# Optimization experiments

Hardware: AMD Instinct MI355X
Metric: run time of the kernel (lower is better)

The kernel has to match this reference:

```python
import jax, jax.numpy as jnp
import numpy as np

TOP_K = 2  # MoEBlock default


def setup_inputs() -> dict:
    key = jax.random.key(0)
    ks = jax.random.split(key, 7)
    B_, S, D, F, E, R = 2, 2048, 1024, 4096, 4, 4
    x  = jax.random.normal(ks[0], (B_, S, D), dtype=jnp.float32)
    Wg = jax.random.normal(ks[1], (E, D), dtype=jnp.float32) * (1.0 / np.sqrt(D))
    bg = jnp.zeros((E,), dtype=jnp.float32)
    Wi = jax.random.normal(ks[2], (F, D), dtype=jnp.float32) * (1.0 / np.sqrt(D))
    Wo = jax.random.normal(ks[3], (D, F), dtype=jnp.float32) * (1.0 / np.sqrt(F))
    A  = jax.random.normal(ks[4], (E, R, D), dtype=jnp.float32) * (1.0 / np.sqrt(D))
    Bm = jax.random.normal(ks[5], (E, F, R), dtype=jnp.float32) * 0.01
    return {"x": x, "Wg": Wg, "bg": bg, "Wi": Wi, "Wo": Wo, "A": A, "B": Bm}


def reference(x, Wg, bg, Wi, Wo, A, B):
    E = Wg.shape[0]
    # ---- Router: softmax gate + top-k ----
    logits = jnp.einsum('bsd,ed->bse', x, Wg) + bg          # [B,S,E]
    scores = jax.nn.softmax(logits, axis=-1)
    topv, topi = jax.lax.top_k(scores, TOP_K)               # [B,S,K]
    # per-token combine weight for each expert (sum of matching top-k probs)
    w = jnp.sum(jax.nn.one_hot(topi, E, dtype=x.dtype) * topv[..., None], axis=-2)  # [B,S,E]
    # ---- Experts: shared frozen FFN + per-expert LoRA (dense, then masked) ----
    base = jnp.einsum('bsd,fd->bsf', x, Wi)                 # shared wi(x), [B,S,F]
    lora_low = jnp.einsum('bsd,erd->bser', x, A)            # [B,S,E,R]
    lora = jnp.einsum('bser,efr->bsef', lora_low, B)        # [B,S,E,F]
    h = jax.nn.relu(base[:, :, None, :] + lora)             # act(wi(x)+lora), [B,S,E,F]
    expert_out = jnp.einsum('bsef,df->bsed', h, Wo)         # wo(.), [B,S,E,D]
    # ---- Combine ----
    out = jnp.einsum('bse,bsed->bsd', w, expert_out)        # [B,S,D]
    return out
```

## Files before the change

kernel.cpp:

```cpp
#include <hip/hip_runtime.h>
#include <stdint.h>

#define BSz 4096
#define Ddim 1024
#define Fdim 4096
#define Edim 4
#define Rdim 4

typedef __attribute__((ext_vector_type(8))) short bf16x8;
typedef __attribute__((ext_vector_type(4))) float f32x4;

__device__ __forceinline__ unsigned short f2bf(float f) {
  union { float f; uint32_t u; } c; c.f = f;
  return (unsigned short)((c.u + 0x7fffu + ((c.u >> 16) & 1u)) >> 16);
}

__global__ __launch_bounds__(256) void zero_f32(float* __restrict__ p, int n4) {
  int i = blockIdx.x * 256 + threadIdx.x;
  if (i < n4) ((float4*)p)[i] = make_float4(0.f, 0.f, 0.f, 0.f);
}

__global__ __launch_bounds__(256) void cvt_kernel(const float* __restrict__ in,
                                                  unsigned short* __restrict__ out,
                                                  int n4) {
  int i = blockIdx.x * 256 + threadIdx.x;
  if (i < n4) {
    float4 v = ((const float4*)in)[i];
    ushort4 o;
    o.x = f2bf(v.x); o.y = f2bf(v.y); o.z = f2bf(v.z); o.w = f2bf(v.w);
    ((ushort4*)out)[i] = o;
  }
}

__global__ __launch_bounds__(256) void router_kernel(const float* __restrict__ x,
                                                     const float* __restrict__ Wg,
                                                     const float* __restrict__ bg,
                                                     const float* __restrict__ Aw,
                                                     float* __restrict__ meta) {
  __shared__ float xs[Ddim];
  __shared__ float dots[Edim + Edim * Rdim];
  const int t = blockIdx.x;
  const float4* xt = (const float4*)(x + (size_t)t * Ddim);
  for (int i = threadIdx.x; i < Ddim / 4; i += 256) ((float4*)xs)[i] = xt[i];
  __syncthreads();
  const int wave = threadIdx.x >> 6, lane = threadIdx.x & 63;
  for (int d = wave * 5; d < wave * 5 + 5; ++d) {
    const float* wrow = (d < Edim) ? (Wg + (size_t)d * Ddim)
                                   : (Aw + (size_t)(d - Edim) * Ddim);
    float s = 0.f;
    for (int i = lane; i < Ddim; i += 64) s += xs[i] * wrow[i];
    for (int off = 32; off; off >>= 1) s += __shfl_down(s, off);
    if (lane == 0) dots[d] = s;
  }
  __syncthreads();
  if (threadIdx.x == 0) {
    float p[Edim];
    float m = -1e30f;
    for (int e = 0; e < Edim; ++e) { p[e] = dots[e] + bg[e]; m = fmaxf(m, p[e]); }
    float sum = 0.f;
    for (int e = 0; e < Edim; ++e) { p[e] = expf(p[e] - m); sum += p[e]; }
    const float inv = 1.f / sum;
    for (int e = 0; e < Edim; ++e) p[e] *= inv;
    int e0 = 0;
    for (int e = 1; e < Edim; ++e) if (p[e] > p[e0]) e0 = e;
    int e1 = (e0 == 0) ? 1 : 0;
    for (int e = 0; e < Edim; ++e) if (e != e0 && p[e] > p[e1]) e1 = e;
    float* mt = meta + (size_t)t * 16;
    mt[0] = (float)e0; mt[1] = (float)e1; mt[2] = p[e0]; mt[3] = p[e1];
    for (int r = 0; r < Rdim; ++r) {
      mt[4 + r] = dots[Edim + e0 * Rdim + r];
      mt[8 + r] = dots[Edim + e1 * Rdim + r];
    }
    mt[12] = 0.f; mt[13] = 0.f; mt[14] = 0.f; mt[15] = 0.f;
  }
}

template <int EPI>
__global__ __launch_bounds__(512, 2)
void gemm256(const unsigned short* __restrict__ Ag,
             const unsigned short* __restrict__ Bg,
             int K, int kslice, int Ncols,
             const float* __restrict__ meta,
             const float* __restrict__ B2,
             unsigned short* __restrict__ outg,
             float* __restrict__ outf) {
  constexpr int BK = 64;
  __shared__ __align__(16) unsigned short sA[2][256 * BK];
  __shared__ __align__(16) unsigned short sB[2][256 * BK];

  const int tid = threadIdx.x;
  const int lane = tid & 63;
  const int wave = tid >> 6;
  const int wm = wave >> 2, wn = wave & 3;
  const int l16 = lane & 15, lhi = lane >> 4;

  const int nwg = gridDim.x * gridDim.y;
  const int lin = blockIdx.y * gridDim.x + blockIdx.x;
  const int cpx = nwg >> 3;
  const int swz = (lin & 7) * cpx + (lin >> 3);
  const int bx = swz % gridDim.x, by = swz / gridDim.x;
  const int bm = by * 256, bn = bx * 256;
  const int kbase = blockIdx.z * kslice;
  const int NT = kslice / BK;

  f32x4 acc[8][4] = {};

  const int srow = tid >> 3;
  const int scol = ((tid & 7) ^ (srow & 7)) * 8;
  const int ldst = tid * 8;

  auto stage = [&](int buf, int kt) {
    const int kof = kbase + kt * BK;
#pragma unroll
    for (int rr = 0; rr < 4; ++rr)
      __builtin_amdgcn_global_load_lds(
          (const __attribute__((address_space(1))) void*)(Ag + (size_t)(bm + srow + rr * 64) * K + kof + scol),
          (__attribute__((address_space(3))) void*)(&sA[buf][ldst + rr * 4096]), 16, 0, 0);
#pragma unroll
    for (int rr = 0; rr < 4; ++rr)
      __builtin_amdgcn_global_load_lds(
          (const __attribute__((address_space(1))) void*)(Bg + (size_t)(bn + srow + rr * 64) * K + kof + scol),
          (__attribute__((address_space(3))) void*)(&sB[buf][ldst + rr * 4096]), 16, 0, 0);
  };

  auto compute = [&](int buf) {
#pragma unroll
    for (int kk = 0; kk < 2; ++kk) {
      bf16x8 af[8], bfv[4];
#pragma unroll
      for (int mi = 0; mi < 8; ++mi) {
        const int r = wm * 128 + mi * 16 + l16;
        af[mi] = *(const bf16x8*)(&sA[buf][r * BK + (((kk * 4 + lhi) ^ (r & 7)) * 8)]);
      }
#pragma unroll
      for (int ni = 0; ni < 4; ++ni) {
        const int r = wn * 64 + ni * 16 + l16;
        bfv[ni] = *(const bf16x8*)(&sB[buf][r * BK + (((kk * 4 + lhi) ^ (r & 7)) * 8)]);
      }
      __builtin_amdgcn_s_setprio(1);
#pragma unroll
      for (int mi = 0; mi < 8; ++mi)
#pragma unroll
        for (int ni = 0; ni < 4; ++ni)
          acc[mi][ni] = __builtin_amdgcn_mfma_f32_16x16x32_bf16(af[mi], bfv[ni], acc[mi][ni], 0, 0, 0);
      __builtin_amdgcn_s_setprio(0);
    }
  };

  stage(0, 0);
  __syncthreads();
  int cur = 0;
  for (int t = 0; t < NT; ++t) {
    if (t + 1 < NT) stage(cur ^ 1, t + 1);
    compute(cur);
    __syncthreads();
    cur ^= 1;
  }

  if (EPI == 0) {
#pragma unroll
    for (int mi = 0; mi < 8; ++mi) {
#pragma unroll
      for (int r = 0; r < 4; ++r) {
        const int row = bm + wm * 128 + mi * 16 + lhi * 4 + r;
        const float* mt = meta + (size_t)row * 16;
        const int e0 = (int)mt[0], e1 = (int)mt[1];
        const float w0 = mt[2], w1 = mt[3];
        const float4 l0 = *(const float4*)(mt + 4);
        const float4 l1 = *(const float4*)(mt + 8);
#pragma unroll
        for (int ni = 0; ni < 4; ++ni) {
          const int f = bn + wn * 64 + ni * 16 + l16;
          const float4 b0 = *(const float4*)(B2 + ((size_t)e0 * Fdim + f) * Rdim);
          const float4 b1 = *(const float4*)(B2 + ((size_t)e1 * Fdim + f) * Rdim);
          const float a = acc[mi][ni][r];
          const float lora0 = l0.x * b0.x + l0.y * b0.y + l0.z * b0.z + l0.w * b0.w;
          const float lora1 = l1.x * b1.x + l1.y * b1.y + l1.z * b1.z + l1.w * b1.w;
          const float gv = w0 * fmaxf(a + lora0, 0.f) + w1 * fmaxf(a + lora1, 0.f);
          outg[(size_t)row * Fdim + f] = f2bf(gv);
        }
      }
    }
  } else {
#pragma unroll
    for (int mi = 0; mi < 8; ++mi)
#pragma unroll
      for (int ni = 0; ni < 4; ++ni)
#pragma unroll
        for (int r = 0; r < 4; ++r) {
          const int row = bm + wm * 128 + mi * 16 + lhi * 4 + r;
          const int col = bn + wn * 64 + ni * 16 + l16;
          unsafeAtomicAdd(&outf[(size_t)row * Ncols + col], acc[mi][ni][r]);
        }
  }
}

extern "C" void kernel_launch(void* const* d_in, const int* in_sizes, int n_in,
                              void* d_out, int out_size, void* d_ws, size_t ws_size,
                              hipStream_t stream) {
  const float* x  = (const float*)d_in[0];
  const float* Wg = (const float*)d_in[1];
  const float* bg = (const float*)d_in[2];
  const float* Wi = (const float*)d_in[3];
  const float* Wo = (const float*)d_in[4];
  const float* Aw = (const float*)d_in[5];
  const float* B2 = (const float*)d_in[6];
  float* out = (float*)d_out;

  unsigned short* xb  = (unsigned short*)d_ws;
  unsigned short* wib = xb  + (size_t)BSz  * Ddim;
  unsigned short* wob = wib + (size_t)Fdim * Ddim;
  unsigned short* g   = wob + (size_t)Ddim * Fdim;
  float* meta = (float*)(g + (size_t)BSz * Fdim);

  zero_f32<<<BSz * Ddim / 4 / 256, 256, 0, stream>>>(out, BSz * Ddim / 4);

  const int n4x = BSz * Ddim / 4;
  cvt_kernel<<<(n4x + 255) / 256, 256, 0, stream>>>(x,  xb,  n4x);
  cvt_kernel<<<(n4x + 255) / 256, 256, 0, stream>>>(Wi, wib, n4x);
  cvt_kernel<<<(n4x + 255) / 256, 256, 0, stream>>>(Wo, wob, n4x);

  router_kernel<<<BSz, 256, 0, stream>>>(x, Wg, bg, Aw, meta);

  gemm256<0><<<dim3(Fdim / 256, BSz / 256, 1), 512, 0, stream>>>(
      xb, wib, Ddim, Ddim, Fdim, meta, B2, g, nullptr);

  gemm256<1><<<dim3(Ddim / 256, BSz / 256, 4), 512, 0, stream>>>(
      g, wob, Fdim, Fdim / 4, Ddim, nullptr, nullptr, nullptr, out);
}
```

Baseline: 200.6 us.

## Replace double-buffered GEMM with 4-stage LDS ring and staged epilogue stores

Replaces the double-buffered BK=64 GEMM with a 4-deep ring of BK=32 tiles. Loads are issued three tiles ahead and waited on with explicit vmcnt counts, and the A/B refills are interleaved between two MFMA half-batches. LDS reads use inline ds_read_b128, and occupancy is lowered to one workgroup per CU. The first GEMM's epilogue now stages bf16 results through LDS so global writes are coalesced 16-byte stores. This aims to hide memory latency better and cut scattered 2-byte stores. The cost is hand-tuned waitcnt logic and lower occupancy, either of which could hurt.

```diff
diff --git a/kernel.cpp b/kernel.cpp
--- a/kernel.cpp
+++ b/kernel.cpp
@@ -13,6 +13,13 @@
 __device__ __forceinline__ unsigned short f2bf(float f) {
   union { float f; uint32_t u; } c; c.f = f;
   return (unsigned short)((c.u + 0x7fffu + ((c.u >> 16) & 1u)) >> 16);
+}
+
+__device__ __forceinline__ bf16x8 ldsr128(const unsigned short* p) {
+  bf16x8 r;
+  unsigned a = (unsigned)(uintptr_t)(const __attribute__((address_space(3))) void*)p;
+  asm volatile("ds_read_b128 %0, %1" : "=v"(r) : "v"(a));
+  return r;
 }
 
 __global__ __launch_bounds__(256) void zero_f32(float* __restrict__ p, int n4) {
@@ -76,17 +83,17 @@
 }
 
 template <int EPI>
-__global__ __launch_bounds__(512, 2)
-void gemm256(const unsigned short* __restrict__ Ag,
-             const unsigned short* __restrict__ Bg,
-             int K, int kslice, int Ncols,
-             const float* __restrict__ meta,
-             const float* __restrict__ B2,
-             unsigned short* __restrict__ outg,
-             float* __restrict__ outf) {
-  constexpr int BK = 64;
-  __shared__ __align__(16) unsigned short sA[2][256 * BK];
-  __shared__ __align__(16) unsigned short sB[2][256 * BK];
+__global__ __launch_bounds__(512, 1)
+void gemmring(const unsigned short* __restrict__ Ag,
+              const unsigned short* __restrict__ Bg,
+              int K, int Ncols,
+              const float* __restrict__ meta,
+              const float* __restrict__ B2,
+              unsigned short* __restrict__ outg,
+              float* __restrict__ outf) {
+  constexpr int BK = 32;
+  constexpr int NT = 32;
+  __shared__ __align__(16) unsigned short lds[65536];
 
   const int tid = threadIdx.x;
   const int lane = tid & 63;
@@ -100,61 +107,87 @@
   const int swz = (lin & 7) * cpx + (lin >> 3);
   const int bx = swz % gridDim.x, by = swz / gridDim.x;
   const int bm = by * 256, bn = bx * 256;
-  const int kbase = blockIdx.z * kslice;
-  const int NT = kslice / BK;
+  const int kbase = blockIdx.z * (NT * BK);
 
   f32x4 acc[8][4] = {};
 
-  const int srow = tid >> 3;
-  const int scol = ((tid & 7) ^ (srow & 7)) * 8;
-  const int ldst = tid * 8;
-
-  auto stage = [&](int buf, int kt) {
-    const int kof = kbase + kt * BK;
-#pragma unroll
-    for (int rr = 0; rr < 4; ++rr)
+  const int srow = tid >> 2;
+  const int scol = ((tid & 3) ^ (srow & 3)) * 8;
+
+  auto stageA = [&](int tt) {
+    unsigned short* dst = lds + (tt & 3) * 8192;
+    const int kof = kbase + tt * BK;
+#pragma unroll
+    for (int rr = 0; rr < 2; ++rr)
       __builtin_amdgcn_global_load_lds(
-          (const __attribute__((address_space(1))) void*)(Ag + (size_t)(bm + srow + rr * 64) * K + kof + scol),
-          (__attribute__((address_space(3))) void*)(&sA[buf][ldst + rr * 4096]), 16, 0, 0);
-#pragma unroll
-    for (int rr = 0; rr < 4; ++rr)
+          (const __attribute__((address_space(1))) void*)(Ag + (size_t)(bm + srow + rr * 128) * K + kof + scol),
+          (__attribute__((address_space(3))) void*)(dst + tid * 8 + rr * 4096), 16, 0, 0);
+  };
+  auto stageB = [&](int tt) {
+    unsigned short* dst = lds + 32768 + (tt & 3) * 8192;
+    const int kof = kbase + tt * BK;
+#pragma unroll
+    for (int rr = 0; rr < 2; ++rr)
       __builtin_amdgcn_global_load_lds(
-          (const __attribute__((address_space(1))) void*)(Bg + (size_t)(bn + srow + rr * 64) * K + kof + scol),
-          (__attribute__((address_space(3))) void*)(&sB[buf][ldst + rr * 4096]), 16, 0, 0);
+          (const __attribute__((address_space(1))) void*)(Bg + (size_t)(bn + srow + rr * 128) * K + kof + scol),
+          (__attribute__((address_space(3))) void*)(dst + tid * 8 + rr * 4096), 16, 0, 0);
   };
 
-  auto compute = [&](int buf) {
-#pragma unroll
-    for (int kk = 0; kk < 2; ++kk) {
-      bf16x8 af[8], bfv[4];
-#pragma unroll
-      for (int mi = 0; mi < 8; ++mi) {
-        const int r = wm * 128 + mi * 16 + l16;
-        af[mi] = *(const bf16x8*)(&sA[buf][r * BK + (((kk * 4 + lhi) ^ (r & 7)) * 8)]);
-      }
-#pragma unroll
-      for (int ni = 0; ni < 4; ++ni) {
-        const int r = wn * 64 + ni * 16 + l16;
-        bfv[ni] = *(const bf16x8*)(&sB[buf][r * BK + (((kk * 4 + lhi) ^ (r & 7)) * 8)]);
-      }
-      __builtin_amdgcn_s_setprio(1);
-#pragma unroll
-      for (int mi = 0; mi < 8; ++mi)
-#pragma unroll
-        for (int ni = 0; ni < 4; ++ni)
-          acc[mi][ni] = __builtin_amdgcn_mfma_f32_16x16x32_bf16(af[mi], bfv[ni], acc[mi][ni], 0, 0, 0);
-      __builtin_amdgcn_s_setprio(0);
-    }
-  };
-
-  stage(0, 0);
-  __syncthreads();
-  int cur = 0;
+  stageA(0); stageB(0);
+  stageA(1); stageB(1);
+  stageA(2); stageB(2);
+
   for (int t = 0; t < NT; ++t) {
-    if (t + 1 < NT) stage(cur ^ 1, t + 1);
-    compute(cur);
-    __syncthreads();
-    cur ^= 1;
+    if (t < NT - 2)       asm volatile("s_waitcnt vmcnt(8)" ::: "memory");
+    else if (t == NT - 2) asm volatile("s_waitcnt vmcnt(4)" ::: "memory");
+    else                  asm volatile("s_waitcnt vmcnt(0)" ::: "memory");
+    __builtin_amdgcn_s_barrier();
+    asm volatile("" ::: "memory");
+
+    const unsigned short* As = lds + (t & 3) * 8192;
+    const unsigned short* Bs = lds + 32768 + (t & 3) * 8192;
+    bf16x8 bfr[4], afr[4];
+
+#pragma unroll
+    for (int ni = 0; ni < 4; ++ni) {
+      const int r = wn * 64 + ni * 16 + l16;
+      bfr[ni] = ldsr128(Bs + r * BK + ((lhi ^ (r & 3)) * 8));
+    }
+#pragma unroll
+    for (int mi = 0; mi < 4; ++mi) {
+      const int r = wm * 128 + mi * 16 + l16;
+      afr[mi] = ldsr128(As + r * BK + ((lhi ^ (r & 3)) * 8));
+    }
+    if (t + 3 < NT) stageA(t + 3);
+    asm volatile("s_waitcnt lgkmcnt(0)" ::: "memory");
+    __builtin_amdgcn_sched_barrier(0);
+    __builtin_amdgcn_s_setprio(1);
+#pragma unroll
+    for (int mi = 0; mi < 4; ++mi)
+#pragma unroll
+      for (int ni = 0; ni < 4; ++ni)
+        acc[mi][ni] = __builtin_amdgcn_mfma_f32_16x16x32_bf16(afr[mi], bfr[ni], acc[mi][ni], 0, 0, 0);
+    __builtin_amdgcn_s_setprio(0);
+
+#pragma unroll
+    for (int mi = 0; mi < 4; ++mi) {
+      const int r = wm * 128 + 64 + mi * 16 + l16;
+      afr[mi] = ldsr128(As + r * BK + ((lhi ^ (r & 3)) * 8));
+    }
+    if (t + 3 < NT) stageB(t + 3);
+    asm volatile("s_waitcnt lgkmcnt(0)" ::: "memory");
+    __builtin_amdgcn_sched_barrier(0);
+    __builtin_amdgcn_s_setprio(1);
+#pragma unroll
+    for (int mi = 0; mi < 4; ++mi)
+#pragma unroll
+      for (int ni = 0; ni < 4; ++ni)
+        acc[4 + mi][ni] = __builtin_amdgcn_mfma_f32_16x16x32_bf16(afr[mi], bfr[ni], acc[4 + mi][ni], 0, 0, 0);
+    __builtin_amdgcn_s_setprio(0);
+
+    asm volatile("" ::: "memory");
+    __builtin_amdgcn_s_barrier();
+    asm volatile("" ::: "memory");
   }
 
   if (EPI == 0) {
@@ -162,7 +195,8 @@
     for (int mi = 0; mi < 8; ++mi) {
 #pragma unroll
       for (int r = 0; r < 4; ++r) {
-        const int row = bm + wm * 128 + mi * 16 + lhi * 4 + r;
+        const int rowl = wm * 128 + mi * 16 + lhi * 4 + r;
+        const int row = bm + rowl;
         const float* mt = meta + (size_t)row * 16;
         const int e0 = (int)mt[0], e1 = (int)mt[1];
         const float w0 = mt[2], w1 = mt[3];
@@ -170,16 +204,26 @@
         const float4 l1 = *(const float4*)(mt + 8);
 #pragma unroll
         for (int ni = 0; ni < 4; ++ni) {
-          const int f = bn + wn * 64 + ni * 16 + l16;
+          const int coll = wn * 64 + ni * 16 + l16;
+          const int f = bn + coll;
           const float4 b0 = *(const float4*)(B2 + ((size_t)e0 * Fdim + f) * Rdim);
           const float4 b1 = *(const float4*)(B2 + ((size_t)e1 * Fdim + f) * Rdim);
           const float a = acc[mi][ni][r];
           const float lora0 = l0.x * b0.x + l0.y * b0.y + l0.z * b0.z + l0.w * b0.w;
           const float lora1 = l1.x * b1.x + l1.y * b1.y + l1.z * b1.z + l1.w * b1.w;
           const float gv = w0 * fmaxf(a + lora0, 0.f) + w1 * fmaxf(a + lora1, 0.f);
-          outg[(size_t)row * Fdim + f] = f2bf(gv);
+          lds[rowl * 256 + coll] = f2bf(gv);
         }
       }
+    }
+    __syncthreads();
+#pragma unroll
+    for (int rnd = 0; rnd < 16; ++rnd) {
+      const int idx = rnd * 512 + tid;
+      const int rowl = idx >> 5;
+      const int chk = idx & 31;
+      *(bf16x8*)(outg + (size_t)(bm + rowl) * Fdim + bn + chk * 8) =
+          *(const bf16x8*)(lds + rowl * 256 + chk * 8);
     }
   } else {
 #pragma unroll
@@ -222,9 +266,9 @@
 
   router_kernel<<<BSz, 256, 0, stream>>>(x, Wg, bg, Aw, meta);
 
-  gemm256<0><<<dim3(Fdim / 256, BSz / 256, 1), 512, 0, stream>>>(
-      xb, wib, Ddim, Ddim, Fdim, meta, B2, g, nullptr);
-
-  gemm256<1><<<dim3(Ddim / 256, BSz / 256, 4), 512, 0, stream>>>(
-      g, wob, Fdim, Fdim / 4, Ddim, nullptr, nullptr, nullptr, out);
-}
+  gemmring<0><<<dim3(Fdim / 256, BSz / 256, 1), 512, 0, stream>>>(
+      xb, wib, Ddim, Fdim, meta, B2, g, nullptr);
+
+  gemmring<1><<<dim3(Ddim / 256, BSz / 256, 4), 512, 0, stream>>>(
+      g, wob, Fdim, Ddim, nullptr, nullptr, nullptr, out);
+}
```

After: 196.0 us. 2.3% less time.
